# Kernel tuning notes

Measured on AMD Instinct MI355X. Metric: run time of the kernel, lower is better.

## Reference

```python
import jax, jax.numpy as jnp
import numpy as np

B, IMG, P, D, E, S, K, L = 2, 512, 16, 384, 768, 16, 4, 12
G = IMG // P
N = G * G  # 1024 patches

def layer_norm(x, w, b):
    m = x.mean(-1, keepdims=True)
    v = ((x - m) ** 2).mean(-1, keepdims=True)
    return (x - m) / jnp.sqrt(v + 1e-5) * w + b

def silu(x):
    return x * jax.nn.sigmoid(x)

def patch_embed(px, w, b, pos):
    Bz = px.shape[0]
    # non-overlapping patchify == stride-P conv with PxP kernel
    x = px.reshape(Bz, 3, G, P, G, P).transpose(0, 2, 4, 1, 3, 5).reshape(Bz, N, 3 * P * P)
    return x @ w.reshape(D, -1).T + b + pos

def mamba_block(x, norm_w, norm_b, in_w, in_b, conv_w, conv_b, xp_w, xp_b, dt_w, dt_b, A, Dp, out_w, out_b):
    res = x
    x = layer_norm(x, norm_w, norm_b)
    xz = x @ in_w.T + in_b                       # (B,N,2E)
    x_main, z = jnp.split(xz, 2, axis=-1)
    # depthwise causal conv (torch pads K-1 both sides then truncates to N == left pad K-1)
    xc = jax.lax.conv_general_dilated(x_main.transpose(0, 2, 1), conv_w, (1,), [(K - 1, 0)],
                                      dimension_numbers=('NCH', 'OIH', 'NCH'), feature_group_count=E)
    xc = silu((xc + conv_b[:, None]).transpose(0, 2, 1))  # (B,N,E)
    xBC = xc @ xp_w.T + xp_b
    xB, xC = jnp.split(xBC, 2, axis=-1)          # each (B,N,S)
    dt = jnp.clip(jax.nn.softplus(xB @ dt_w.T + dt_b), 1e-4, 1.0)    # (B,N,E)
    dA = jnp.exp(jnp.clip(dt[..., None] * A[None, None], -20.0, 0.0))  # (B,N,E,S)

    def step(h, inp):
        dA_i, xB_i, xC_i, xc_i = inp             # (B,E,S),(B,S),(B,S),(B,E)
        h = dA_i * h + xB_i[:, None, :] * xc_i[:, :, None]
        return h, jnp.einsum('bes,bs->be', h, xC_i)

    h0 = jnp.zeros((x.shape[0], E, S), x.dtype)
    _, ys = jax.lax.scan(step, h0, (dA.transpose(1, 0, 2, 3), xB.transpose(1, 0, 2),
                                    xC.transpose(1, 0, 2), xc.transpose(1, 0, 2)))
    y = ys.transpose(1, 0, 2)                    # (B,N,E)
    y = (y + Dp * xc) * silu(z)
    return res + y @ out_w.T + out_b

def setup_inputs() -> dict:
    key = jax.random.key(0)
    ks = jax.random.split(key, 10)
    rnd = lambda k, shape, s=0.02: jax.random.normal(k, shape, jnp.float32) * s
    return {
        'pixel_values': jax.random.normal(ks[0], (B, 3, IMG, IMG), jnp.float32),
        'patch_w': rnd(ks[1], (D, 3, P, P)),
        'patch_b': jnp.zeros((D,), jnp.float32),
        'pos_embed': rnd(ks[2], (1, N, D)),
        'norm_w': jnp.ones((L, D), jnp.float32), 'norm_b': jnp.zeros((L, D), jnp.float32),
        'in_w': rnd(ks[3], (L, 2 * E, D)), 'in_b': jnp.zeros((L, 2 * E), jnp.float32),
        'conv_w': rnd(ks[4], (L, E, 1, K), 0.3), 'conv_b': jnp.zeros((L, E), jnp.float32),
        'xp_w': rnd(ks[5], (L, 2 * S, E)), 'xp_b': jnp.zeros((L, 2 * S), jnp.float32),
        'dt_w': rnd(ks[6], (L, E, S), 0.1), 'dt_b': jnp.zeros((L, E), jnp.float32),
        'A': -jnp.tile(jnp.arange(1, S + 1, dtype=jnp.float32), (L, E, 1)),
        'Dp': jnp.ones((L, E), jnp.float32),
        'out_w': rnd(ks[7], (L, D, E)), 'out_b': jnp.zeros((L, D), jnp.float32),
        'fnorm_w': jnp.ones((D,), jnp.float32), 'fnorm_b': jnp.zeros((D,), jnp.float32),
        'scale_w': rnd(ks[8], (3, D, D)), 'scale_b': jnp.zeros((3, D), jnp.float32),
    }

def reference(pixel_values, patch_w, patch_b, pos_embed, norm_w, norm_b, in_w, in_b,
              conv_w, conv_b, xp_w, xp_b, dt_w, dt_b, A, Dp, out_w, out_b,
              fnorm_w, fnorm_b, scale_w, scale_b):
    x = patch_embed(pixel_values, patch_w, patch_b, pos_embed)
    layers_per_scale = L // 3
    scales = []
    for i in range(L):
        x = mamba_block(x, norm_w[i], norm_b[i], in_w[i], in_b[i], conv_w[i], conv_b[i],
                        xp_w[i], xp_b[i], dt_w[i], dt_b[i], A[i], Dp[i], out_w[i], out_b[i])
        if i % layers_per_scale == 0 and i // layers_per_scale < 3:
            j = i // layers_per_scale
            scales.append(x @ scale_w[j].T + scale_b[j])
    feats = layer_norm(x, fnorm_w, fnorm_b)
    # stacked: [features, scale_4, scale_8, scale_16] -> (4, B, N, D)
    return jnp.stack([feats] + scales)
```

## Files before the change

kernel.cpp:

```cpp
#include <hip/hip_runtime.h>
#include <hip/hip_bf16.h>

constexpr int Bz = 2, IMG = 512, Pp = 16, D = 384, E = 768, S = 16, L = 12;
constexpr int G = IMG / Pp;
constexpr int Np = G * G;
constexpr int M = Bz * Np;
constexpr int TWO_E = 2 * E;

typedef short bf16x8 __attribute__((ext_vector_type(8)));
typedef float fx4    __attribute__((ext_vector_type(4)));

static __device__ __forceinline__ unsigned short f2bf(float f){
  unsigned int u = __float_as_uint(f);
  u = (u + 0x7FFFu + ((u >> 16) & 1u)) >> 16;
  return (unsigned short)u;
}
static __device__ __forceinline__ float bf2f(unsigned short h){
  return __uint_as_float(((unsigned int)h) << 16);
}

static __device__ __forceinline__ float fexp2(float x){
  float r;
  asm("v_exp_f32 %0, %1" : "=v"(r) : "v"(x));
  return r;
}

static __device__ __forceinline__ float quad_sum(float v){
  int a = __builtin_amdgcn_update_dpp(0, __float_as_int(v), 0xB1, 0xF, 0xF, true);
  v += __int_as_float(a);
  int b = __builtin_amdgcn_update_dpp(0, __float_as_int(v), 0x4E, 0xF, 0xF, true);
  v += __int_as_float(b);
  return v;
}

constexpr size_t PW_N = (size_t)D * 768;
constexpr size_t IW_N = (size_t)L * TWO_E * D;
constexpr size_t OW_N = (size_t)L * D * E;
constexpr size_t SW_N = (size_t)3 * D * D;
__device__ short g_pw_h[PW_N], g_pw_l[PW_N];
__device__ short g_iw_h[IW_N], g_iw_l[IW_N];
__device__ short g_ow_h[OW_N], g_ow_l[OW_N];
__device__ short g_swx_h[SW_N], g_swx_l[SW_N];

__global__ void convw_kernel(const float* __restrict__ pw, const float* __restrict__ iw,
                             const float* __restrict__ ow, const float* __restrict__ sw){
  size_t i = (size_t)blockIdx.x * 256 + threadIdx.x;
  if (i >= PW_N + IW_N + OW_N + SW_N) return;
  const float* src; short *dh, *dl; size_t j = i;
  if (j < PW_N){ src = pw; dh = g_pw_h; dl = g_pw_l; }
  else if ((j -= PW_N) < IW_N){ src = iw; dh = g_iw_h; dl = g_iw_l; }
  else if ((j -= IW_N) < OW_N){ src = ow; dh = g_ow_h; dl = g_ow_l; }
  else { j -= OW_N; src = sw; dh = g_swx_h; dl = g_swx_l; }
  float f = src[j];
  unsigned short h = f2bf(f);
  dh[j] = (short)h; dl[j] = (short)f2bf(f - bf2f(h));
}

__global__ void patchify_kernel(const float* __restrict__ px,
                                short* __restrict__ oh, short* __restrict__ ol){
  int idx = blockIdx.x * 256 + threadIdx.x;
  if (idx >= M * 768) return;
  int k = idx % 768, m = idx / 768;
  int b = m / Np, n = m % Np;
  int gy = n / G, gx = n % G;
  int c = k / (Pp * Pp), r = k % (Pp * Pp);
  int py = r / Pp, pxi = r % Pp;
  size_t src = ((size_t)(b * 3 + c) * IMG + gy * Pp + py) * IMG + gx * Pp + pxi;
  float f = px[src];
  unsigned short h = f2bf(f);
  oh[idx] = (short)h; ol[idx] = (short)f2bf(f - bf2f(h));
}

__global__ __launch_bounds__(256)
void layernorm_bf(const float* __restrict__ x, const float* __restrict__ w,
                  const float* __restrict__ bb, short* __restrict__ oh,
                  short* __restrict__ ol){
  int wave = threadIdx.x >> 6, lane = threadIdx.x & 63;
  int row = blockIdx.x * 4 + wave;
  const float* xr = x + (size_t)row * D;
  float v[6], s = 0.f, sq = 0.f;
  #pragma unroll
  for (int i = 0; i < 6; i++){ v[i] = xr[lane + 64 * i]; s += v[i]; sq += v[i] * v[i]; }
  #pragma unroll
  for (int off = 32; off; off >>= 1){ s += __shfl_xor(s, off); sq += __shfl_xor(sq, off); }
  float mean = s * (1.f / D);
  float var  = sq * (1.f / D) - mean * mean;
  float inv  = 1.0f / sqrtf(var + 1e-5f);
  #pragma unroll
  for (int i = 0; i < 6; i++){
    int c = lane + 64 * i;
    float o = (v[i] - mean) * inv * w[c] + bb[c];
    unsigned short h = f2bf(o);
    oh[(size_t)row * D + c] = (short)h;
    ol[(size_t)row * D + c] = (short)f2bf(o - bf2f(h));
  }
}

__global__ __launch_bounds__(256)
void layernorm_f32(const float* __restrict__ x, const float* __restrict__ w,
                   const float* __restrict__ bb, float* __restrict__ outf){
  int wave = threadIdx.x >> 6, lane = threadIdx.x & 63;
  int row = blockIdx.x * 4 + wave;
  const float* xr = x + (size_t)row * D;
  float v[6], s = 0.f, sq = 0.f;
  #pragma unroll
  for (int i = 0; i < 6; i++){ v[i] = xr[lane + 64 * i]; s += v[i]; sq += v[i] * v[i]; }
  #pragma unroll
  for (int off = 32; off; off >>= 1){ s += __shfl_xor(s, off); sq += __shfl_xor(sq, off); }
  float mean = s * (1.f / D);
  float var  = sq * (1.f / D) - mean * mean;
  float inv  = 1.0f / sqrtf(var + 1e-5f);
  #pragma unroll
  for (int i = 0; i < 6; i++){
    int c = lane + 64 * i;
    outf[(size_t)row * D + c] = (v[i] - mean) * inv * w[c] + bb[c];
  }
}

__global__ __launch_bounds__(256)
void gemm_in(const short* __restrict__ Ah, const short* __restrict__ Al,
             size_t woff, const float* __restrict__ bias,
             float* __restrict__ C, float* __restrict__ C2){
  constexpr int BKp = 40;
  __shared__ __align__(16) short sAh[64 * BKp],  sAl[64 * BKp];
  __shared__ __align__(16) short sWh[128 * BKp], sWl[128 * BKp];
  const short* Wh = g_iw_h + woff;
  const short* Wl = g_iw_l + woff;
  const int t = threadIdx.x, wid = t >> 6, lane = t & 63;
  const int m0 = blockIdx.y * 64, n0 = blockIdx.x * 128;
  const int wn = wid * 32;

  fx4 acc[4][2];
  #pragma unroll
  for (int a = 0; a < 4; a++)
    #pragma unroll
    for (int b = 0; b < 2; b++)
      #pragma unroll
      for (int i = 0; i < 4; i++) acc[a][b][i] = 0.f;

  const int rA = t >> 2, kpA = (t & 3) << 3;
  const int rW = t >> 1, kpW = (t & 1) << 4;
  const int row = lane & 15, kq = lane >> 4;

  for (int kt = 0; kt < D; kt += 32){
    *(bf16x8*)&sAh[rA * BKp + kpA] = *(const bf16x8*)(Ah + (size_t)(m0 + rA) * D + kt + kpA);
    *(bf16x8*)&sAl[rA * BKp + kpA] = *(const bf16x8*)(Al + (size_t)(m0 + rA) * D + kt + kpA);
    *(bf16x8*)&sWh[rW * BKp + kpW]     = *(const bf16x8*)(Wh + (size_t)(n0 + rW) * D + kt + kpW);
    *(bf16x8*)&sWh[rW * BKp + kpW + 8] = *(const bf16x8*)(Wh + (size_t)(n0 + rW) * D + kt + kpW + 8);
    *(bf16x8*)&sWl[rW * BKp + kpW]     = *(const bf16x8*)(Wl + (size_t)(n0 + rW) * D + kt + kpW);
    *(bf16x8*)&sWl[rW * BKp + kpW + 8] = *(const bf16x8*)(Wl + (size_t)(n0 + rW) * D + kt + kpW + 8);
    __syncthreads();
    bf16x8 ah[4], al[4], bh[2], bl[2];
    #pragma unroll
    for (int tm = 0; tm < 4; tm++){
      ah[tm] = *(const bf16x8*)&sAh[(tm * 16 + row) * BKp + kq * 8];
      al[tm] = *(const bf16x8*)&sAl[(tm * 16 + row) * BKp + kq * 8];
    }
    #pragma unroll
    for (int tn = 0; tn < 2; tn++){
      bh[tn] = *(const bf16x8*)&sWh[(wn + tn * 16 + row) * BKp + kq * 8];
      bl[tn] = *(const bf16x8*)&sWl[(wn + tn * 16 + row) * BKp + kq * 8];
    }
    #pragma unroll
    for (int tm = 0; tm < 4; tm++)
      #pragma unroll
      for (int tn = 0; tn < 2; tn++){
        acc[tm][tn] = __builtin_amdgcn_mfma_f32_16x16x32_bf16(ah[tm], bh[tn], acc[tm][tn], 0, 0, 0);
        acc[tm][tn] = __builtin_amdgcn_mfma_f32_16x16x32_bf16(ah[tm], bl[tn], acc[tm][tn], 0, 0, 0);
        acc[tm][tn] = __builtin_amdgcn_mfma_f32_16x16x32_bf16(al[tm], bh[tn], acc[tm][tn], 0, 0, 0);
      }
    __syncthreads();
  }

  const int row4 = (lane >> 4) * 4, coln = lane & 15;
  #pragma unroll
  for (int tm = 0; tm < 4; tm++)
    #pragma unroll
    for (int tn = 0; tn < 2; tn++){
      int n = n0 + wn + tn * 16 + coln;
      int mb = m0 + tm * 16 + row4;
      float4 v4;
      float* vp = (float*)&v4;
      #pragma unroll
      for (int i = 0; i < 4; i++) vp[i] = acc[tm][tn][i] + bias[n];
      if (n < E){
        *(float4*)&C[(size_t)n * M + mb] = v4;
      } else {
        #pragma unroll
        for (int i = 0; i < 4; i++){
          float sig = 1.f / (1.f + expf(-vp[i]));
          vp[i] = vp[i] * sig;
        }
        *(float4*)&C2[(size_t)(n - E) * M + mb] = v4;
      }
    }
}

__global__ __launch_bounds__(256)
void gemm_patch(const short* __restrict__ Ah, const short* __restrict__ Al,
                const float* __restrict__ bias, float* __restrict__ C,
                const float* __restrict__ pos){
  constexpr int BKp = 40;
  __shared__ __align__(16) short sAh[64 * BKp], sAl[64 * BKp];
  __shared__ __align__(16) short sWh[64 * BKp], sWl[64 * BKp];
  const int t = threadIdx.x, wid = t >> 6, lane = t & 63;
  const int m0 = blockIdx.y * 64, n0 = blockIdx.x * 64;

  fx4 acc[4];
  #pragma unroll
  for (int a = 0; a < 4; a++)
    #pragma unroll
    for (int i = 0; i < 4; i++) acc[a][i] = 0.f;

  const int r = t >> 2, kp = (t & 3) << 3;
  const int row = lane & 15, kq = lane >> 4;

  for (int kt = 0; kt < 768; kt += 32){
    *(bf16x8*)&sAh[r * BKp + kp] = *(const bf16x8*)(Ah + (size_t)(m0 + r) * 768 + kt + kp);
    *(bf16x8*)&sAl[r * BKp + kp] = *(const bf16x8*)(Al + (size_t)(m0 + r) * 768 + kt + kp);
    *(bf16x8*)&sWh[r * BKp + kp] = *(const bf16x8*)(g_pw_h + (size_t)(n0 + r) * 768 + kt + kp);
    *(bf16x8*)&sWl[r * BKp + kp] = *(const bf16x8*)(g_pw_l + (size_t)(n0 + r) * 768 + kt + kp);
    __syncthreads();
    bf16x8 bh = *(const bf16x8*)&sWh[(wid * 16 + row) * BKp + kq * 8];
    bf16x8 bl = *(const bf16x8*)&sWl[(wid * 16 + row) * BKp + kq * 8];
    #pragma unroll
    for (int tm = 0; tm < 4; tm++){
      bf16x8 ah = *(const bf16x8*)&sAh[(tm * 16 + row) * BKp + kq * 8];
      bf16x8 al = *(const bf16x8*)&sAl[(tm * 16 + row) * BKp + kq * 8];
      acc[tm] = __builtin_amdgcn_mfma_f32_16x16x32_bf16(ah, bh, acc[tm], 0, 0, 0);
      acc[tm] = __builtin_amdgcn_mfma_f32_16x16x32_bf16(ah, bl, acc[tm], 0, 0, 0);
      acc[tm] = __builtin_amdgcn_mfma_f32_16x16x32_bf16(al, bh, acc[tm], 0, 0, 0);
    }
    __syncthreads();
  }

  const int row4 = (lane >> 4) * 4, coln = lane & 15;
  #pragma unroll
  for (int tm = 0; tm < 4; tm++){
    int n = n0 + wid * 16 + coln;
    int mb = m0 + tm * 16 + row4;
    #pragma unroll
    for (int i = 0; i < 4; i++){
      int m = mb + i;
      C[(size_t)m * D + n] = acc[tm][i] + bias[n] + pos[(size_t)(m & (Np - 1)) * D + n];
    }
  }
}

__global__ __launch_bounds__(256)
void gemm_scale(const float* __restrict__ A, size_t woff,
                const float* __restrict__ bias, float* __restrict__ C){
  constexpr int BKp = 40;
  __shared__ __align__(16) short sAh[64 * BKp], sAl[64 * BKp];
  __shared__ __align__(16) short sWh[64 * BKp], sWl[64 * BKp];
  const short* Wh = g_swx_h + woff;
  const short* Wl = g_swx_l + woff;
  const int t = threadIdx.x, wid = t >> 6, lane = t & 63;
  const int m0 = blockIdx.y * 64, n0 = blockIdx.x * 64;

  fx4 acc[4];
  #pragma unroll
  for (int a = 0; a < 4; a++)
    #pragma unroll
    for (int i = 0; i < 4; i++) acc[a][i] = 0.f;

  const int r = t >> 2, kp = (t & 3) << 3;
  const int row = lane & 15, kq = lane >> 4;

  for (int kt = 0; kt < D; kt += 32){
    {
      const float* ap = A + (size_t)(m0 + r) * D + kt + kp;
      float4 f0 = *(const float4*)ap, f1 = *(const float4*)(ap + 4);
      float f[8] = {f0.x, f0.y, f0.z, f0.w, f1.x, f1.y, f1.z, f1.w};
      short hh[8], ll[8];
      #pragma unroll
      for (int i = 0; i < 8; i++){
        unsigned short h = f2bf(f[i]);
        hh[i] = (short)h; ll[i] = (short)f2bf(f[i] - bf2f(h));
      }
      *(bf16x8*)&sAh[r * BKp + kp] = *(bf16x8*)hh;
      *(bf16x8*)&sAl[r * BKp + kp] = *(bf16x8*)ll;
    }
    *(bf16x8*)&sWh[r * BKp + kp] = *(const bf16x8*)(Wh + (size_t)(n0 + r) * D + kt + kp);
    *(bf16x8*)&sWl[r * BKp + kp] = *(const bf16x8*)(Wl + (size_t)(n0 + r) * D + kt + kp);
    __syncthreads();
    bf16x8 bh = *(const bf16x8*)&sWh[(wid * 16 + row) * BKp + kq * 8];
    bf16x8 bl = *(const bf16x8*)&sWl[(wid * 16 + row) * BKp + kq * 8];
    #pragma unroll
    for (int tm = 0; tm < 4; tm++){
      bf16x8 ah = *(const bf16x8*)&sAh[(tm * 16 + row) * BKp + kq * 8];
      bf16x8 al = *(const bf16x8*)&sAl[(tm * 16 + row) * BKp + kq * 8];
      acc[tm] = __builtin_amdgcn_mfma_f32_16x16x32_bf16(ah, bh, acc[tm], 0, 0, 0);
      acc[tm] = __builtin_amdgcn_mfma_f32_16x16x32_bf16(ah, bl, acc[tm], 0, 0, 0);
      acc[tm] = __builtin_amdgcn_mfma_f32_16x16x32_bf16(al, bh, acc[tm], 0, 0, 0);
    }
    __syncthreads();
  }

  const int row4 = (lane >> 4) * 4, coln = lane & 15;
  #pragma unroll
  for (int tm = 0; tm < 4; tm++){
    int n = n0 + wid * 16 + coln;
    int mb = m0 + tm * 16 + row4;
    #pragma unroll
    for (int i = 0; i < 4; i++){
      int m = mb + i;
      C[(size_t)m * D + n] = acc[tm][i] + bias[n];
    }
  }
}

__global__ __launch_bounds__(256)
void gemm_bf_at(const short* __restrict__ ATh, const short* __restrict__ ATl, int K,
                size_t woff, const float* __restrict__ bias,
                float* __restrict__ C, int ncols, float* __restrict__ zbuf){
  constexpr int BKp = 40;
  __shared__ __align__(16) short sAh[64 * BKp], sAl[64 * BKp];
  __shared__ __align__(16) short sWh[64 * BKp], sWl[64 * BKp];
  const short* Wh = g_ow_h + woff;
  const short* Wl = g_ow_l + woff;
  const int t = threadIdx.x, wid = t >> 6, lane = t & 63;
  const int m0 = blockIdx.y * 64, n0 = blockIdx.x * 64;

  fx4 acc[4];
  #pragma unroll
  for (int a = 0; a < 4; a++)
    #pragma unroll
    for (int i = 0; i < 4; i++) acc[a][i] = 0.f;

  const int rw = t >> 2, kpw = (t & 3) << 3;
  const int kr2 = (t & 15) * 2, mc4 = (t >> 4) * 4;
  const int row = lane & 15, kq = lane >> 4;

  for (int kt = 0; kt < K; kt += 32){
    {
      const uint2 h0 = *(const uint2*)(ATh + (size_t)(kt + kr2) * M + m0 + mc4);
      const uint2 h1 = *(const uint2*)(ATh + (size_t)(kt + kr2 + 1) * M + m0 + mc4);
      const uint2 l0 = *(const uint2*)(ATl + (size_t)(kt + kr2) * M + m0 + mc4);
      const uint2 l1 = *(const uint2*)(ATl + (size_t)(kt + kr2 + 1) * M + m0 + mc4);
      const unsigned int h0a[2] = {h0.x, h0.y}, h1a[2] = {h1.x, h1.y};
      const unsigned int l0a[2] = {l0.x, l0.y}, l1a[2] = {l1.x, l1.y};
      #pragma unroll
      for (int j = 0; j < 4; j++){
        unsigned int s0 = (h0a[j >> 1] >> ((j & 1) * 16)) & 0xFFFFu;
        unsigned int s1 = (h1a[j >> 1] >> ((j & 1) * 16)) & 0xFFFFu;
        *(unsigned int*)&sAh[(mc4 + j) * BKp + kr2] = s0 | (s1 << 16);
        unsigned int t0 = (l0a[j >> 1] >> ((j & 1) * 16)) & 0xFFFFu;
        unsigned int t1 = (l1a[j >> 1] >> ((j & 1) * 16)) & 0xFFFFu;
        *(unsigned int*)&sAl[(mc4 + j) * BKp + kr2] = t0 | (t1 << 16);
      }
    }
    *(bf16x8*)&sWh[rw * BKp + kpw] = *(const bf16x8*)(Wh + (size_t)(n0 + rw) * K + kt + kpw);
    *(bf16x8*)&sWl[rw * BKp + kpw] = *(const bf16x8*)(Wl + (size_t)(n0 + rw) * K + kt + kpw);
    __syncthreads();
    bf16x8 bh = *(const bf16x8*)&sWh[(wid * 16 + row) * BKp + kq * 8];
    bf16x8 bl = *(const bf16x8*)&sWl[(wid * 16 + row) * BKp + kq * 8];
    #pragma unroll
    for (int tm = 0; tm < 4; tm++){
      bf16x8 ah = *(const bf16x8*)&sAh[(tm * 16 + row) * BKp + kq * 8];
      bf16x8 al = *(const bf16x8*)&sAl[(tm * 16 + row) * BKp + kq * 8];
      acc[tm] = __builtin_amdgcn_mfma_f32_16x16x32_bf16(ah, bh, acc[tm], 0, 0, 0);
      acc[tm] = __builtin_amdgcn_mfma_f32_16x16x32_bf16(ah, bl, acc[tm], 0, 0, 0);
      acc[tm] = __builtin_amdgcn_mfma_f32_16x16x32_bf16(al, bh, acc[tm], 0, 0, 0);
    }
    __syncthreads();
  }

  const int row4 = (lane >> 4) * 4, coln = lane & 15;
  #pragma unroll
  for (int tm = 0; tm < 4; tm++)
    #pragma unroll
    for (int i = 0; i < 4; i++){
      int m = m0 + tm * 16 + row4 + i;
      int n = n0 + wid * 16 + coln;
      float v = acc[tm][i] + bias[n] + C[(size_t)m * ncols + n];
      C[(size_t)m * ncols + n] = v;
    }

  int gid = blockIdx.y * gridDim.x + blockIdx.x;
  int idx = gid * 256 + t;
  if (idx < M * 16)
    *(float2*)&zbuf[idx * 2] = make_float2(0.f, 0.f);
}

__global__ __launch_bounds__(256)
void gemm_xp(const float* __restrict__ xcT, const float* __restrict__ W,
             const float* __restrict__ bias, float* __restrict__ C){
  __shared__ float As[16][64 + 1];
  __shared__ float Ws[16][32 + 1];
  int tid = threadIdx.x;
  int tx = tid & 15, ty = tid >> 4;
  int m0 = blockIdx.y * 64, kb = blockIdx.x * 192;
  float acc[4][2];
  #pragma unroll
  for (int i = 0; i < 4; i++){ acc[i][0] = 0.f; acc[i][1] = 0.f; }
  for (int kt = kb; kt < kb + 192; kt += 16){
    #pragma unroll
    for (int ps = 0; ps < 4; ps++){
      int rr = (tid >> 6) + 4 * ps, mc = tid & 63;
      As[rr][mc] = xcT[(size_t)(kt + rr) * M + m0 + mc];
    }
    if (tid < 128){
      int c = tid >> 2, kk = (tid & 3) << 2;
      const float* wp = W + (size_t)c * E + kt + kk;
      Ws[kk + 0][c] = wp[0]; Ws[kk + 1][c] = wp[1];
      Ws[kk + 2][c] = wp[2]; Ws[kk + 3][c] = wp[3];
    }
    __syncthreads();
    #pragma unroll
    for (int k = 0; k < 16; k++){
      float a[4], w[2];
      #pragma unroll
      for (int i = 0; i < 4; i++) a[i] = As[k][ty * 4 + i];
      w[0] = Ws[k][tx * 2]; w[1] = Ws[k][tx * 2 + 1];
      #pragma unroll
      for (int i = 0; i < 4; i++){ acc[i][0] += a[i] * w[0]; acc[i][1] += a[i] * w[1]; }
    }
    __syncthreads();
  }
  #pragma unroll
  for (int i = 0; i < 4; i++){
    int m = m0 + ty * 4 + i;
    #pragma unroll
    for (int j = 0; j < 2; j++){
      int n = tx * 2 + j;
      float v = acc[i][j];
      if (blockIdx.x == 0) v += bias[n];
      atomicAdd(&C[(size_t)m * 32 + n], v);
    }
  }
}

__global__ __launch_bounds__(256)
void conv_silu_t(const float* __restrict__ xmT, const float* __restrict__ cw,
                 const float* __restrict__ cb, float* __restrict__ xcT){
  const int e = blockIdx.x, t = threadIdx.x;
  const float w0 = cw[e * 4], w1 = cw[e * 4 + 1], w2 = cw[e * 4 + 2], w3 = cw[e * 4 + 3];
  const float bias = cb[e];
  const float* src = xmT + (size_t)e * M;
  float* dst = xcT + (size_t)e * M;
  int mb = t * 8;
  #pragma unroll
  for (int j = 0; j < 8; j++){
    int m = mb + j, n = m & (Np - 1);
    float acc = bias + w3 * src[m];
    if (n >= 1) acc += w2 * src[m - 1];
    if (n >= 2) acc += w1 * src[m - 2];
    if (n >= 3) acc += w0 * src[m - 3];
    float sig = 1.f / (1.f + expf(-acc));
    dst[m] = acc * sig;
  }
}

__global__ __launch_bounds__(256)
void scan_kernel(const float* __restrict__ xcT, const float* __restrict__ zst,
                 const float* __restrict__ xBC,
                 const float* __restrict__ Aptr, const float* __restrict__ Dp,
                 const float* __restrict__ dt_w, const float* __restrict__ dt_b,
                 short* __restrict__ yh, short* __restrict__ yl){
  __shared__ float sdx[2176];
  __shared__ float sHin[64 * 16];
  __shared__ float scr[2048];
  const int t = threadIdx.x;
  const int c = t >> 2;
  const int u = t & 3;
  const int r = blockIdx.x, b = r / E, e = r % E;
  const int bNp = b * Np;
  const float dpe = Dp[e];
  constexpr float LOG2E = 1.4426950408889634f;
  float4 a4 = *(const float4*)(Aptr + e * S + u * 4);
  const float a20 = a4.x * LOG2E, a21 = a4.y * LOG2E, a22 = a4.z * LOG2E, a23 = a4.w * LOG2E;
  const float* xcp = xcT + (size_t)e * M + bNp;
  const float* zsp = zst + (size_t)e * M + bNp;

  {
    const float* dw = dt_w + e * 16;
    float4 w0 = *(const float4*)dw,       w1 = *(const float4*)(dw + 4);
    float4 w2 = *(const float4*)(dw + 8), w3 = *(const float4*)(dw + 12);
    float db = dt_b[e];
    #pragma unroll
    for (int p = 0; p < 4; p++){
      int q = t + p * 256;
      const float* xb = xBC + (size_t)(bNp + q) * 32;
      float4 a0 = *(const float4*)xb,       a1 = *(const float4*)(xb + 4);
      float4 a2 = *(const float4*)(xb + 8), a3 = *(const float4*)(xb + 12);
      float v = db + a0.x * w0.x + a0.y * w0.y + a0.z * w0.z + a0.w * w0.w
                   + a1.x * w1.x + a1.y * w1.y + a1.z * w1.z + a1.w * w1.w
                   + a2.x * w2.x + a2.y * w2.y + a2.z * w2.z + a2.w * w2.w
                   + a3.x * w3.x + a3.y * w3.y + a3.z * w3.z + a3.w * w3.w;
      v = (v > 15.f) ? v : log1pf(expf(v));
      v = fminf(fmaxf(v, 1e-4f), 1.0f);
      int w = (q << 1) + ((q >> 4) << 1);
      *(float2*)&sdx[w] = make_float2(v, xcp[q]);
    }
  }
  __syncthreads();

  const int pos0 = c * 16;
  const int wbase = (pos0 << 1) + ((pos0 >> 4) << 1);
  const float* xbp  = xBC + ((size_t)(bNp + pos0) * 32 + u * 4);
  const float* xcsp = xbp + 16;

  float h0 = 0.f, h1 = 0.f, h2 = 0.f, h3 = 0.f, sdt = 0.f;
  #pragma unroll
  for (int i = 0; i < 16; i++){
    float2 dx = *(const float2*)&sdx[wbase + 2 * i];
    float4 xb = *(const float4*)(xbp + (size_t)i * 32);
    float dt = dx.x, xcv = dx.y;
    sdt += dt;
    float e0 = fexp2(dt * a20), e1 = fexp2(dt * a21);
    float e2 = fexp2(dt * a22), e3 = fexp2(dt * a23);
    h0 = e0 * h0 + xb.x * xcv;
    h1 = e1 * h1 + xb.y * xcv;
    h2 = e2 * h2 + xb.z * xcv;
    h3 = e3 * h3 + xb.w * xcv;
  }
  {
    float p0 = fexp2(sdt * a20), p1 = fexp2(sdt * a21);
    float p2 = fexp2(sdt * a22), p3 = fexp2(sdt * a23);
    *(float4*)&scr[c * 16 + u * 4]        = make_float4(h0, h1, h2, h3);
    *(float4*)&scr[1024 + c * 16 + u * 4] = make_float4(p0, p1, p2, p3);
  }
  __syncthreads();

  if (t < 16){
    float H = 0.f;
    #pragma unroll 8
    for (int cc = 0; cc < 64; cc++){
      sHin[cc * 16 + t] = H;
      H = scr[1024 + cc * 16 + t] * H + scr[cc * 16 + t];
    }
  }
  __syncthreads();

  {
    float4 hin = *(const float4*)&sHin[c * 16 + u * 4];
    h0 = hin.x; h1 = hin.y; h2 = hin.z; h3 = hin.w;
  }
  float* yloc = scr;
  const int ybase = pos0 + ((pos0 >> 4) << 2);
  #pragma unroll
  for (int i = 0; i < 16; i++){
    float2 dx = *(const float2*)&sdx[wbase + 2 * i];
    float4 xb  = *(const float4*)(xbp  + (size_t)i * 32);
    float4 xcs = *(const float4*)(xcsp + (size_t)i * 32);
    float dt = dx.x, xcv = dx.y;
    float e0 = fexp2(dt * a20), e1 = fexp2(dt * a21);
    float e2 = fexp2(dt * a22), e3 = fexp2(dt * a23);
    h0 = e0 * h0 + xb.x * xcv;
    h1 = e1 * h1 + xb.y * xcv;
    h2 = e2 * h2 + xb.z * xcv;
    h3 = e3 * h3 + xb.w * xcv;
    float yp = h0 * xcs.x + h1 * xcs.y + h2 * xcs.z + h3 * xcs.w;
    yp = quad_sum(yp);
    if (u == 0) yloc[ybase + i] = yp;
  }
  __syncthreads();

  {
    int n4 = t * 4;
    float4 z4 = *(const float4*)&zsp[n4];
    const float* zp = (const float*)&z4;
    int yb = n4 + ((n4 >> 4) << 2);
    int xw = (n4 << 1) + ((n4 >> 4) << 1);
    unsigned int hpack[2], lpack[2];
    #pragma unroll
    for (int half = 0; half < 2; half++){
      unsigned int hp = 0, lp = 0;
      #pragma unroll
      for (int j = 0; j < 2; j++){
        int jj = half * 2 + j;
        float xcv = sdx[xw + 2 * jj + 1];
        float val = (yloc[yb + jj] + dpe * xcv) * zp[jj];
        unsigned short hh = f2bf(val);
        unsigned short ll = f2bf(val - bf2f(hh));
        hp |= ((unsigned int)hh) << (16 * j);
        lp |= ((unsigned int)ll) << (16 * j);
      }
      hpack[half] = hp; lpack[half] = lp;
    }
    size_t o = (size_t)e * M + bNp + n4;
    *(uint2*)&yh[o] = make_uint2(hpack[0], hpack[1]);
    *(uint2*)&yl[o] = make_uint2(lpack[0], lpack[1]);
  }
}

extern "C" void kernel_launch(void* const* d_in, const int* in_sizes, int n_in,
                              void* d_out, int out_size, void* d_ws, size_t ws_size,
                              hipStream_t stream){
  const float* px      = (const float*)d_in[0];
  const float* patch_w = (const float*)d_in[1];
  const float* patch_b = (const float*)d_in[2];
  const float* pos     = (const float*)d_in[3];
  const float* norm_w  = (const float*)d_in[4];
  const float* norm_b  = (const float*)d_in[5];
  const float* in_w    = (const float*)d_in[6];
  const float* in_b    = (const float*)d_in[7];
  const float* conv_w  = (const float*)d_in[8];
  const float* conv_b  = (const float*)d_in[9];
  const float* xp_w    = (const float*)d_in[10];
  const float* xp_b    = (const float*)d_in[11];
  const float* dt_w    = (const float*)d_in[12];
  const float* dt_b    = (const float*)d_in[13];
  const float* Aab     = (const float*)d_in[14];
  const float* Dp      = (const float*)d_in[15];
  const float* out_w   = (const float*)d_in[16];
  const float* out_b   = (const float*)d_in[17];
  const float* fnorm_w = (const float*)d_in[18];
  const float* fnorm_b = (const float*)d_in[19];
  const float* scale_w = (const float*)d_in[20];
  const float* scale_b = (const float*)d_in[21];
  float* out = (float*)d_out;

  float* x   = (float*)d_ws;
  float* xmT = x + (size_t)M * D;
  float* zst = xmT + (size_t)M * E;
  float* xcT = zst + (size_t)M * E;
  float* xBC = xcT + (size_t)M * E;
  short* xnh = (short*)(xBC + (size_t)M * 32);
  short* xnl = xnh + (size_t)M * D;
  short* yh  = (short*)xmT;
  short* yl  = yh + (size_t)M * E;
  short* pbh = yh, *pbl = yl;

  constexpr size_t TOTW = PW_N + IW_N + OW_N + SW_N;
  convw_kernel<<<(int)((TOTW + 255) / 256), 256, 0, stream>>>(patch_w, in_w, out_w, scale_w);
  hipMemsetAsync(xBC, 0, (size_t)M * 32 * sizeof(float), stream);

  patchify_kernel<<<(M * 768 + 255) / 256, 256, 0, stream>>>(px, pbh, pbl);
  gemm_patch<<<dim3(D / 64, M / 64), 256, 0, stream>>>(pbh, pbl, patch_b, x, pos);

  for (int l = 0; l < L; l++){
    layernorm_bf<<<M / 4, 256, 0, stream>>>(x, norm_w + l * D, norm_b + l * D, xnh, xnl);
    gemm_in<<<dim3(TWO_E / 128, M / 64), 256, 0, stream>>>(
        xnh, xnl, (size_t)l * TWO_E * D, in_b + l * TWO_E, xmT, zst);
    conv_silu_t<<<E, 256, 0, stream>>>(
        xmT, conv_w + (size_t)l * E * 4, conv_b + l * E, xcT);
    gemm_xp<<<dim3(4, M / 64), 256, 0, stream>>>(
        xcT, xp_w + (size_t)l * 32 * E, xp_b + l * 32, xBC);
    scan_kernel<<<Bz * E, 256, 0, stream>>>(
        xcT, zst, xBC, Aab + (size_t)l * E * S, Dp + l * E,
        dt_w + (size_t)l * E * S, dt_b + l * E, yh, yl);
    gemm_bf_at<<<dim3(D / 64, M / 64), 256, 0, stream>>>(
        yh, yl, E, (size_t)l * D * E, out_b + l * D, x, D, xBC);
    if (l % 4 == 0 && l / 4 < 3){
      int j = l / 4;
      gemm_scale<<<dim3(D / 64, M / 64), 256, 0, stream>>>(
          x, (size_t)j * D * D, scale_b + j * D, out + (size_t)(1 + j) * M * D);
    }
  }
  layernorm_f32<<<M / 4, 256, 0, stream>>>(x, fnorm_w, fnorm_b, out);
}
```

Baseline: 1.555 ms.

## Fuse dt projection into scan pass and use wave-shuffle chunk prefix scan

The dt projection and softplus move from a separate prologue into the first scan pass. Each quad of threads now computes a partial dot product and reduces it with DPP, and softplus uses hardware exp2/log2. The serial 64-step cross-chunk carry loop run by 16 threads is replaced by a shuffle-based Hillis-Steele scan within each wavefront plus a short cross-wave prefix through shared memory. This removes two block barriers and the serial bottleneck, and hoists the z load earlier, at the cost of extra shuffles and dropping the large-v softplus shortcut (possible overflow of exp2 for very large v).

```diff
diff --git a/kernel.cpp b/kernel.cpp
--- a/kernel.cpp
+++ b/kernel.cpp
@@ -22,6 +22,11 @@
 static __device__ __forceinline__ float fexp2(float x){
   float r;
   asm("v_exp_f32 %0, %1" : "=v"(r) : "v"(x));
+  return r;
+}
+static __device__ __forceinline__ float flog2(float x){
+  float r;
+  asm("v_log_f32 %0, %1" : "=v"(r) : "v"(x));
   return r;
 }
 
@@ -459,85 +464,96 @@
                  const float* __restrict__ dt_w, const float* __restrict__ dt_b,
                  short* __restrict__ yh, short* __restrict__ yl){
   __shared__ float sdx[2176];
-  __shared__ float sHin[64 * 16];
-  __shared__ float scr[2048];
+  __shared__ float yloc[1280];
+  __shared__ float swt[4][16][2];
   const int t = threadIdx.x;
+  const int lane = t & 63;
+  const int w = t >> 6;
   const int c = t >> 2;
+  const int cl = c & 15;
   const int u = t & 3;
   const int r = blockIdx.x, b = r / E, e = r % E;
   const int bNp = b * Np;
   const float dpe = Dp[e];
-  constexpr float LOG2E = 1.4426950408889634f;
+  constexpr float LOG2E  = 1.4426950408889634f;
+  constexpr float RLOG2E = 0.6931471805599453f;
   float4 a4 = *(const float4*)(Aptr + e * S + u * 4);
   const float a20 = a4.x * LOG2E, a21 = a4.y * LOG2E, a22 = a4.z * LOG2E, a23 = a4.w * LOG2E;
+  float4 dtw4 = *(const float4*)(dt_w + e * 16 + u * 4);
+  const float db = dt_b[e];
   const float* xcp = xcT + (size_t)e * M + bNp;
   const float* zsp = zst + (size_t)e * M + bNp;
 
-  {
-    const float* dw = dt_w + e * 16;
-    float4 w0 = *(const float4*)dw,       w1 = *(const float4*)(dw + 4);
-    float4 w2 = *(const float4*)(dw + 8), w3 = *(const float4*)(dw + 12);
-    float db = dt_b[e];
-    #pragma unroll
-    for (int p = 0; p < 4; p++){
-      int q = t + p * 256;
-      const float* xb = xBC + (size_t)(bNp + q) * 32;
-      float4 a0 = *(const float4*)xb,       a1 = *(const float4*)(xb + 4);
-      float4 a2 = *(const float4*)(xb + 8), a3 = *(const float4*)(xb + 12);
-      float v = db + a0.x * w0.x + a0.y * w0.y + a0.z * w0.z + a0.w * w0.w
-                   + a1.x * w1.x + a1.y * w1.y + a1.z * w1.z + a1.w * w1.w
-                   + a2.x * w2.x + a2.y * w2.y + a2.z * w2.z + a2.w * w2.w
-                   + a3.x * w3.x + a3.y * w3.y + a3.z * w3.z + a3.w * w3.w;
-      v = (v > 15.f) ? v : log1pf(expf(v));
-      v = fminf(fmaxf(v, 1e-4f), 1.0f);
-      int w = (q << 1) + ((q >> 4) << 1);
-      *(float2*)&sdx[w] = make_float2(v, xcp[q]);
-    }
-  }
-  __syncthreads();
-
   const int pos0 = c * 16;
-  const int wbase = (pos0 << 1) + ((pos0 >> 4) << 1);
+  const int wbase = 34 * c;
   const float* xbp  = xBC + ((size_t)(bNp + pos0) * 32 + u * 4);
   const float* xcsp = xbp + 16;
 
   float h0 = 0.f, h1 = 0.f, h2 = 0.f, h3 = 0.f, sdt = 0.f;
+  float4 xcv4;
   #pragma unroll
   for (int i = 0; i < 16; i++){
-    float2 dx = *(const float2*)&sdx[wbase + 2 * i];
+    if ((i & 3) == 0) xcv4 = *(const float4*)(xcp + pos0 + i);
     float4 xb = *(const float4*)(xbp + (size_t)i * 32);
-    float dt = dx.x, xcv = dx.y;
-    sdt += dt;
-    float e0 = fexp2(dt * a20), e1 = fexp2(dt * a21);
-    float e2 = fexp2(dt * a22), e3 = fexp2(dt * a23);
+    float xcv = ((const float*)&xcv4)[i & 3];
+    float part = xb.x * dtw4.x + xb.y * dtw4.y + xb.z * dtw4.z + xb.w * dtw4.w;
+    float v = quad_sum(part) + db;
+    v = flog2(1.f + fexp2(v * LOG2E)) * RLOG2E;
+    v = fminf(fmaxf(v, 1e-4f), 1.0f);
+    sdt += v;
+    if (u == 0) *(float2*)&sdx[wbase + 2 * i] = make_float2(v, xcv);
+    float e0 = fexp2(v * a20), e1 = fexp2(v * a21);
+    float e2 = fexp2(v * a22), e3 = fexp2(v * a23);
     h0 = e0 * h0 + xb.x * xcv;
     h1 = e1 * h1 + xb.y * xcv;
     h2 = e2 * h2 + xb.z * xcv;
     h3 = e3 * h3 + xb.w * xcv;
   }
+  float P0 = fexp2(sdt * a20), P1 = fexp2(sdt * a21);
+  float P2 = fexp2(sdt * a22), P3 = fexp2(sdt * a23);
+
+  #pragma unroll
+  for (int st = 1; st <= 8; st <<= 1){
+    int sl = (cl >= st) ? (lane - 4 * st) : lane;
+    float q0 = __shfl(h0, sl), g0 = __shfl(P0, sl);
+    float q1 = __shfl(h1, sl), g1 = __shfl(P1, sl);
+    float q2 = __shfl(h2, sl), g2 = __shfl(P2, sl);
+    float q3 = __shfl(h3, sl), g3 = __shfl(P3, sl);
+    if (cl >= st){
+      h0 = P0 * q0 + h0; P0 *= g0;
+      h1 = P1 * q1 + h1; P1 *= g1;
+      h2 = P2 * q2 + h2; P2 *= g2;
+      h3 = P3 * q3 + h3; P3 *= g3;
+    }
+  }
+  if (cl == 15){
+    swt[w][u * 4 + 0][0] = h0; swt[w][u * 4 + 0][1] = P0;
+    swt[w][u * 4 + 1][0] = h1; swt[w][u * 4 + 1][1] = P1;
+    swt[w][u * 4 + 2][0] = h2; swt[w][u * 4 + 2][1] = P2;
+    swt[w][u * 4 + 3][0] = h3; swt[w][u * 4 + 3][1] = P3;
+  }
+  __syncthreads();
+  float pre0 = 0.f, pre1 = 0.f, pre2 = 0.f, pre3 = 0.f;
+  for (int ww = 0; ww < w; ww++){
+    pre0 = swt[ww][u * 4 + 0][1] * pre0 + swt[ww][u * 4 + 0][0];
+    pre1 = swt[ww][u * 4 + 1][1] * pre1 + swt[ww][u * 4 + 1][0];
+    pre2 = swt[ww][u * 4 + 2][1] * pre2 + swt[ww][u * 4 + 2][0];
+    pre3 = swt[ww][u * 4 + 3][1] * pre3 + swt[ww][u * 4 + 3][0];
+  }
   {
-    float p0 = fexp2(sdt * a20), p1 = fexp2(sdt * a21);
-    float p2 = fexp2(sdt * a22), p3 = fexp2(sdt * a23);
-    *(float4*)&scr[c * 16 + u * 4]        = make_float4(h0, h1, h2, h3);
-    *(float4*)&scr[1024 + c * 16 + u * 4] = make_float4(p0, p1, p2, p3);
-  }
-  __syncthreads();
-
-  if (t < 16){
-    float H = 0.f;
-    #pragma unroll 8
-    for (int cc = 0; cc < 64; cc++){
-      sHin[cc * 16 + t] = H;
-      H = scr[1024 + cc * 16 + t] * H + scr[cc * 16 + t];
-    }
-  }
-  __syncthreads();
-
-  {
-    float4 hin = *(const float4*)&sHin[c * 16 + u * 4];
-    h0 = hin.x; h1 = hin.y; h2 = hin.z; h3 = hin.w;
-  }
-  float* yloc = scr;
+    int sl = (cl >= 1) ? (lane - 4) : lane;
+    float he0 = __shfl(h0, sl), pe0 = __shfl(P0, sl);
+    float he1 = __shfl(h1, sl), pe1 = __shfl(P1, sl);
+    float he2 = __shfl(h2, sl), pe2 = __shfl(P2, sl);
+    float he3 = __shfl(h3, sl), pe3 = __shfl(P3, sl);
+    h0 = (cl == 0) ? pre0 : (pe0 * pre0 + he0);
+    h1 = (cl == 0) ? pre1 : (pe1 * pre1 + he1);
+    h2 = (cl == 0) ? pre2 : (pe2 * pre2 + he2);
+    h3 = (cl == 0) ? pre3 : (pe3 * pre3 + he3);
+  }
+
+  float4 z4 = *(const float4*)&zsp[t * 4];
+
   const int ybase = pos0 + ((pos0 >> 4) << 2);
   #pragma unroll
   for (int i = 0; i < 16; i++){
@@ -559,7 +575,6 @@
 
   {
     int n4 = t * 4;
-    float4 z4 = *(const float4*)&zsp[n4];
     const float* zp = (const float*)&z4;
     int yb = n4 + ((n4 >> 4) << 2);
     int xw = (n4 << 1) + ((n4 >> 4) << 1);
```

Result: no change. 1.572 ms (+1.1%).
